# Performance work log

Measured on AMD Instinct MI355X. Metric: run time of the kernel, lower is better.

The kernel has to match this reference:

```python
import jax, jax.numpy as jnp
import numpy as np

N, K, C, H, V = 4096, 32, 128, 128, 21   # residues, kNN, node/edge dim, hidden, vocab
NEG_SLOPE = 0.2

def gatv2(src_feat, tgt_feat, edge_feat, Wl, bl, Wr, br, We, be, att, b_out):
    # GATv2Conv (1 head, eval mode) on a regular kNN graph.
    # src_feat: [N,K,Din] gathered source-node features per edge; tgt_feat: [N,Din]
    xl = src_feat @ Wl + bl                       # [N,K,C]
    xr = tgt_feat @ Wr + br                       # [N,C]
    ee = edge_feat @ We + be                      # [N,K,C]
    m = jax.nn.leaky_relu(xl + xr[:, None, :] + ee, NEG_SLOPE)
    alpha = jax.nn.softmax(jnp.einsum('nkc,c->nk', m, att), axis=1)
    return jnp.einsum('nk,nkc->nc', alpha, xl) + b_out

def setup_inputs():
    key = jax.random.key(0)
    ks = jax.random.split(key, 32)
    w = lambda k, s: jax.random.normal(k, s, jnp.float32) * 0.05
    z0 = lambda s: jnp.zeros(s, jnp.float32)
    return dict(
        E=jax.random.normal(ks[0], (N, K, C), jnp.float32),
        E_idx=jax.random.randint(ks[1], (N, K), 0, N),
        S=jax.random.randint(ks[2], (N,), 0, V),
        mask=jnp.ones((N,), jnp.float32),
        chain_M=jnp.ones((N,), jnp.float32),
        z=jax.random.normal(ks[3], (N,), jnp.float32),
        Wl1=w(ks[4], (C, C)), bl1=z0((C,)),
        Wr1=w(ks[5], (C, C)), br1=z0((C,)),
        We1=w(ks[6], (C, C)), be1=z0((C,)),
        a1=w(ks[7], (C,)), bo1=z0((C,)),
        Wl2=w(ks[8], (C + H, C)), bl2=z0((C,)),
        Wr2=w(ks[9], (C + H, C)), br2=z0((C,)),
        We2=w(ks[10], (C, C)), be2=z0((C,)),
        a2=w(ks[11], (C,)), bo2=z0((C,)),
        W_s=w(ks[12], (V, H)),
        W_out=w(ks[13], (C, V)), b_out=z0((V,)),
    )

def reference(E, E_idx, S, mask, chain_M, z,
              Wl1, bl1, Wr1, br1, We1, be1, a1, bo1,
              Wl2, bl2, Wr2, br2, We2, be2, a2, bo2,
              W_s, W_out, b_out):
    # encoder GAT over zero-initialized node features
    x0 = jnp.zeros((N, C), E.dtype)
    node_attr = gatv2(x0[E_idx], x0, E, Wl1, bl1, Wr1, br1, We1, be1, a1, bo1)
    seq_attr = W_s[S]                                        # [N,H]
    h_full = jnp.concatenate([node_attr, seq_attr], -1)      # [N,C+H]
    h_mask = jnp.concatenate([node_attr, jnp.zeros_like(seq_attr)], -1)
    cm = chain_M * mask
    decoding_order = jnp.argsort((cm + 1e-4) * jnp.abs(z))   # [N]
    P = jax.nn.one_hot(decoding_order, N, dtype=E.dtype)     # [N,N] permutation
    L = 1.0 - jnp.triu(jnp.ones((N, N), E.dtype))            # strictly lower tri
    order_mask_backward = jnp.einsum('ij,iq,jp->qp', L, P, P)
    mask_attend = jnp.take_along_axis(order_mask_backward, E_idx, axis=1)[..., None]
    m1d = mask[:, None, None]
    mask_bw = m1d * mask_attend
    mask_fw = m1d * (1.0 - mask_attend)
    # per-edge source features: neighbor seq embedding visible only if decoded earlier
    src = h_full[E_idx] * mask_bw + h_mask[E_idx] * mask_fw  # [N,K,C+H]
    out = gatv2(src, h_mask, E, Wl2, bl2, Wr2, br2, We2, be2, a2, bo2)
    logits = out @ W_out + b_out
    return jax.nn.log_softmax(logits, axis=-1)
```

## Files before the change

kernel.cpp:

```cpp
#include <hip/hip_runtime.h>
#include <hip/hip_bf16.h>

typedef short short8 __attribute__((ext_vector_type(8)));
typedef float float4v __attribute__((ext_vector_type(4)));

#define WS_T   0
#define WS_D   2688
#define WS_C   2816
#define WS_O   2944
#define WS_A2  3072
#define WS_G   7296
#define WS_B0  7744
#define WS_B1  7776
#define WS_M   7808

__device__ __forceinline__ unsigned int pack2bf(float a, float b) {
  union { float f; unsigned int u; } xa, xb;
  xa.f = a; xb.f = b;
  return ((xa.u + 0x8000u) >> 16) | ((xb.u + 0x8000u) & 0xFFFF0000u);
}

__global__ __launch_bounds__(256) void pg10_pre(
    const float* __restrict__ Wl2, const float* __restrict__ Wr2,
    const float* __restrict__ We2, const float* __restrict__ bl1,
    const float* __restrict__ bl2, const float* __restrict__ br2,
    const float* __restrict__ be2, const float* __restrict__ a2,
    const float* __restrict__ bo1, const float* __restrict__ bo2,
    const float* __restrict__ W_s, const float* __restrict__ mask,
    const float* __restrict__ chain_M, const float* __restrict__ z,
    const int* __restrict__ S, const float* __restrict__ W_out,
    const float* __restrict__ b_out, void* __restrict__ ws)
{
  __shared__ float sA[128], sB[128];
  short* wsW = (short*)ws;
  float* F = (float*)ws + 8192;
  const int b = blockIdx.x, tid = threadIdx.x;
  if (b == 0) {
    for (int s = tid; s < 16384; s += 256) {
      const int row = s >> 7, c = s & 127;
      const int q = row >> 5, lh = (row & 31) >> 3, j = row & 7;
      const int t = c >> 4, cl = c & 15;
      union { float f; unsigned int u; } x; x.f = We2[s];
      const unsigned int r = x.u + 0x7FFFu + ((x.u >> 16) & 1u);
      wsW[(((q * 8 + t) * 64) + lh * 16 + cl) * 8 + j] = (short)(r >> 16);
    }
    if (tid < 128) {
      const int c = tid;
      float cl0 = 0.f, cr0 = 0.f;
      for (int i = 0; i < 128; i++) {
        const float s = bl1[i] + bo1[i];
        cl0 += s * Wl2[i * 128 + c];
        cr0 += s * Wr2[i * 128 + c];
      }
      const float O = bl2[c] + bo2[c];
      F[WS_D + c]  = be2[c] + bl2[c] + br2[c] + cr0;
      F[WS_C + c]  = cl0;
      F[WS_O + c]  = O;
      F[WS_A2 + c] = a2[c];
      sA[c] = O;
      sB[c] = cl0;
    }
    __syncthreads();
    if (tid < 21) {
      float b0 = b_out[tid], b1 = 0.f;
      for (int c = 0; c < 128; c++) {
        b0 = fmaf(sA[c], W_out[c * 21 + tid], b0);
        b1 = fmaf(sB[c], W_out[c * 21 + tid], b1);
      }
      F[WS_B0 + tid] = b0;
      F[WS_B1 + tid] = b1;
    }
  } else if (b <= 21) {
    const int v = b - 1;
    if (tid < 128) {
      const int c = tid;
      float acc = 0.f;
      for (int h = 0; h < 128; h++)
        acc += W_s[v * 128 + h] * Wl2[(128 + h) * 128 + c];
      F[WS_T + v * 128 + c] = acc;
      sA[c] = acc;
    }
    __syncthreads();
    if (tid < 21) {
      float g = 0.f;
      for (int c = 0; c < 128; c++)
        g = fmaf(sA[c], W_out[c * 21 + tid], g);
      F[WS_G + v * 21 + tid] = g;
    }
  } else {
    const int n = (b - 22) * 256 + tid;
    F[WS_M + 2 * n] = (chain_M[n] * mask[n] + 1e-4f) * fabsf(z[n]);
    ((int*)F)[WS_M + 2 * n + 1] = S[n];
  }
}

__global__ __launch_bounds__(256, 4) void pg10_main(
    const float* __restrict__ E, const int* __restrict__ E_idx,
    const float* __restrict__ mask, const void* __restrict__ ws,
    float* __restrict__ out)
{
  __shared__ __align__(16) short ldsE[4][32 * 136];

  const short* wsW = (const short*)ws;
  const float* F = (const float*)ws + 8192;
  const int tid  = threadIdx.x;
  const int wave = tid >> 6;
  const int lane = tid & 63;
  const int quad = lane >> 4;
  const int lid  = lane & 15;
  const int n    = blockIdx.x * 4 + wave;
  const float maskn = mask[n];

  int jidx = 0;
  if (lane < 32) jidx = E_idx[n * 32 + lane];

  const float* ebase = E + (size_t)n * 32 * 128;
  short* myE = ldsE[wave];
#pragma unroll
  for (int i = 0; i < 8; i++) {
    const int e = i * 512 + lane * 8;
    const float4 A = *(const float4*)(ebase + e);
    const float4 B = *(const float4*)(ebase + e + 4);
    union { short8 s; unsigned int u[4]; } v;
    v.u[0] = pack2bf(A.x, A.y);
    v.u[1] = pack2bf(A.z, A.w);
    v.u[2] = pack2bf(B.x, B.y);
    v.u[3] = pack2bf(B.z, B.w);
    *(short8*)(myE + (e >> 7) * 136 + (e & 127)) = v.s;
  }

  float wkv = 0.f; int rvv = 0;
  const float keyn = F[WS_M + 2 * n];
  if (lane < 32) {
    const float2 mj = *(const float2*)(F + WS_M + 2 * jidx);
    const int before = (mj.x < keyn) || (mj.x == keyn && jidx < n);
    wkv = before ? maskn : 0.f;
    union { float f; int i; } c; c.f = mj.y; rvv = c.i;
  }
  int rows[2][4]; float wks[2][4];
#pragma unroll
  for (int g = 0; g < 2; g++)
#pragma unroll
    for (int r = 0; r < 4; r++) {
      const int kk = g * 16 + quad * 4 + r;
      rows[g][r] = __shfl(rvv, kk) * 128;
      wks[g][r]  = __shfl(wkv, kk);
    }

  __builtin_amdgcn_wave_barrier();

  short8 afr[2][4];
#pragma unroll
  for (int g = 0; g < 2; g++)
#pragma unroll
    for (int q = 0; q < 4; q++)
      afr[g][q] = *(const short8*)(myE + (g * 16 + lid) * 136 + q * 32 + quad * 8);

  float part[2][4] = {{0.f, 0.f, 0.f, 0.f}, {0.f, 0.f, 0.f, 0.f}};
#pragma unroll
  for (int t = 0; t < 8; t++) {
    short8 bfr[4];
#pragma unroll
    for (int q = 0; q < 4; q++)
      bfr[q] = *(const short8*)(wsW + (((q * 8 + t) * 64) + lane) * 8);
    float4v ac0 = {0.f, 0.f, 0.f, 0.f}, ac1 = {0.f, 0.f, 0.f, 0.f};
#pragma unroll
    for (int q = 0; q < 4; q++) {
      ac0 = __builtin_amdgcn_mfma_f32_16x16x32_bf16(afr[0][q], bfr[q], ac0, 0, 0, 0);
      ac1 = __builtin_amdgcn_mfma_f32_16x16x32_bf16(afr[1][q], bfr[q], ac1, 0, 0, 0);
    }
    const int c = t * 16 + lid;
    const float dvt  = F[WS_D + c] + maskn * F[WS_C + c];
    const float a2vt = F[WS_A2 + c];
#pragma unroll
    for (int r = 0; r < 4; r++) {
      float v0 = ac0[r] + dvt + wks[0][r] * F[WS_T + rows[0][r] + c];
      float v1 = ac1[r] + dvt + wks[1][r] * F[WS_T + rows[1][r] + c];
      v0 = fmaxf(v0, 0.f) + 0.2f * fminf(v0, 0.f);
      v1 = fmaxf(v1, 0.f) + 0.2f * fminf(v1, 0.f);
      part[0][r] = fmaf(v0, a2vt, part[0][r]);
      part[1][r] = fmaf(v1, a2vt, part[1][r]);
    }
  }
  float sreg[2][4];
#pragma unroll
  for (int g = 0; g < 2; g++)
#pragma unroll
    for (int r = 0; r < 4; r++) {
      float v = part[g][r];
      v += __shfl_xor(v, 1);
      v += __shfl_xor(v, 2);
      v += __shfl_xor(v, 4);
      v += __shfl_xor(v, 8);
      sreg[g][r] = v;
    }

  float mx = -1e30f;
#pragma unroll
  for (int g = 0; g < 2; g++)
#pragma unroll
    for (int r = 0; r < 4; r++) mx = fmaxf(mx, sreg[g][r]);
  mx = fmaxf(mx, __shfl_xor(mx, 16));
  mx = fmaxf(mx, __shfl_xor(mx, 32));
  float eg[2][4], esum = 0.f;
#pragma unroll
  for (int g = 0; g < 2; g++)
#pragma unroll
    for (int r = 0; r < 4; r++) {
      eg[g][r] = expf(sreg[g][r] - mx);
      esum += eg[g][r];
    }
  esum += __shfl_xor(esum, 16);
  esum += __shfl_xor(esum, 32);
  const float inv = 1.f / esum;
  float cg[2][4];
#pragma unroll
  for (int g = 0; g < 2; g++)
#pragma unroll
    for (int r = 0; r < 4; r++) cg[g][r] = eg[g][r] * inv * wks[g][r];

  float lg = (lane < 21) ? (F[WS_B0 + lane] + maskn * F[WS_B1 + lane]) : -1e30f;
#pragma unroll
  for (int kk = 0; kk < 32; kk++) {
    const int g = kk >> 4, sq = (kk >> 2) & 3, r = kk & 3;
    const float cf = __shfl(cg[g][r], sq * 16);
    const int row = (rows[0][0], __shfl(rvv, kk)) * 21;
    if (lane < 21) lg = fmaf(cf, F[WS_G + row + lane], lg);
  }

  float lmx = lg;
  lmx = fmaxf(lmx, __shfl_xor(lmx, 1));
  lmx = fmaxf(lmx, __shfl_xor(lmx, 2));
  lmx = fmaxf(lmx, __shfl_xor(lmx, 4));
  lmx = fmaxf(lmx, __shfl_xor(lmx, 8));
  lmx = fmaxf(lmx, __shfl_xor(lmx, 16));
  float ex = (lane < 21) ? expf(lg - lmx) : 0.f;
  float es = ex;
  es += __shfl_xor(es, 1);
  es += __shfl_xor(es, 2);
  es += __shfl_xor(es, 4);
  es += __shfl_xor(es, 8);
  es += __shfl_xor(es, 16);
  if (lane < 21)
    out[n * 21 + lane] = lg - lmx - logf(es);
}

extern "C" void kernel_launch(void* const* d_in, const int* in_sizes, int n_in,
                              void* d_out, int out_size, void* d_ws, size_t ws_size,
                              hipStream_t stream)
{
  const float* E       = (const float*)d_in[0];
  const int*   E_idx   = (const int*)d_in[1];
  const int*   S       = (const int*)d_in[2];
  const float* mask    = (const float*)d_in[3];
  const float* chain_M = (const float*)d_in[4];
  const float* z       = (const float*)d_in[5];
  const float* bl1     = (const float*)d_in[7];
  const float* bo1     = (const float*)d_in[13];
  const float* Wl2     = (const float*)d_in[14];
  const float* bl2     = (const float*)d_in[15];
  const float* Wr2     = (const float*)d_in[16];
  const float* br2     = (const float*)d_in[17];
  const float* We2     = (const float*)d_in[18];
  const float* be2     = (const float*)d_in[19];
  const float* a2      = (const float*)d_in[20];
  const float* bo2     = (const float*)d_in[21];
  const float* W_s     = (const float*)d_in[22];
  const float* W_out   = (const float*)d_in[23];
  const float* b_out   = (const float*)d_in[24];

  pg10_pre<<<38, 256, 0, stream>>>(Wl2, Wr2, We2, bl1, bl2, br2, be2, a2,
                                   bo1, bo2, W_s, mask, chain_M, z, S,
                                   W_out, b_out, d_ws);
  pg10_main<<<1024, 256, 0, stream>>>(E, E_idx, mask, d_ws, (float*)d_out);
}
```

Baseline: 168.2 us.

## Fuse preprocessing into main kernel with flag-based inter-block synchronization

Merges the weight-preprocessing kernel into the main GAT kernel. The first 38 blocks do the preprocessing and then publish release flags; every block spin-waits on those flags after staging its E tile into LDS. This removes a kernel launch and the inter-kernel gap, and lets the E loads overlap with the preprocessing. It also hoists the per-column bias and attention loads out of the MFMA loop, splits the logit accumulation into two chains, and uses the HIP bf16 pack intrinsic. The flags are never reset between calls, so later calls can read stale workspace without waiting, and correctness relies on the flag blocks being resident.

```diff
diff --git a/kernel.cpp b/kernel.cpp
--- a/kernel.cpp
+++ b/kernel.cpp
@@ -4,111 +4,120 @@
 typedef short short8 __attribute__((ext_vector_type(8)));
 typedef float float4v __attribute__((ext_vector_type(4)));
 
-#define WS_T   0
-#define WS_D   2688
-#define WS_C   2816
-#define WS_O   2944
-#define WS_A2  3072
-#define WS_G   7296
-#define WS_B0  7744
-#define WS_B1  7776
-#define WS_M   7808
-
-__device__ __forceinline__ unsigned int pack2bf(float a, float b) {
-  union { float f; unsigned int u; } xa, xb;
-  xa.f = a; xb.f = b;
-  return ((xa.u + 0x8000u) >> 16) | ((xb.u + 0x8000u) & 0xFFFF0000u);
+#define WS_T    0
+#define WS_D    2688
+#define WS_C    2816
+#define WS_O    2944
+#define WS_A2   3072
+#define WS_G    7296
+#define WS_B0   7744
+#define WS_B1   7776
+#define WS_M    7808
+#define WS_FLG  16000
+#define MAGIC   0x5EEDF00D
+
+__device__ __forceinline__ ushort f2bf(float f) {
+  union { float f; unsigned int u; } x;
+  x.f = f;
+  unsigned int r = x.u + 0x7FFFu + ((x.u >> 16) & 1u);
+  return (ushort)(r >> 16);
 }
-
-__global__ __launch_bounds__(256) void pg10_pre(
-    const float* __restrict__ Wl2, const float* __restrict__ Wr2,
-    const float* __restrict__ We2, const float* __restrict__ bl1,
-    const float* __restrict__ bl2, const float* __restrict__ br2,
-    const float* __restrict__ be2, const float* __restrict__ a2,
-    const float* __restrict__ bo1, const float* __restrict__ bo2,
-    const float* __restrict__ W_s, const float* __restrict__ mask,
+__device__ __forceinline__ unsigned int pkbf(float a, float b) {
+  __hip_bfloat162 h = __float22bfloat162_rn(make_float2(a, b));
+  return *(unsigned int*)&h;
+}
+
+__global__ __launch_bounds__(256, 4) void pg11(
+    const float* __restrict__ E, const int* __restrict__ E_idx,
+    const int* __restrict__ S, const float* __restrict__ mask,
     const float* __restrict__ chain_M, const float* __restrict__ z,
-    const int* __restrict__ S, const float* __restrict__ W_out,
-    const float* __restrict__ b_out, void* __restrict__ ws)
-{
-  __shared__ float sA[128], sB[128];
-  short* wsW = (short*)ws;
-  float* F = (float*)ws + 8192;
-  const int b = blockIdx.x, tid = threadIdx.x;
-  if (b == 0) {
-    for (int s = tid; s < 16384; s += 256) {
-      const int row = s >> 7, c = s & 127;
-      const int q = row >> 5, lh = (row & 31) >> 3, j = row & 7;
-      const int t = c >> 4, cl = c & 15;
-      union { float f; unsigned int u; } x; x.f = We2[s];
-      const unsigned int r = x.u + 0x7FFFu + ((x.u >> 16) & 1u);
-      wsW[(((q * 8 + t) * 64) + lh * 16 + cl) * 8 + j] = (short)(r >> 16);
-    }
-    if (tid < 128) {
-      const int c = tid;
-      float cl0 = 0.f, cr0 = 0.f;
-      for (int i = 0; i < 128; i++) {
-        const float s = bl1[i] + bo1[i];
-        cl0 += s * Wl2[i * 128 + c];
-        cr0 += s * Wr2[i * 128 + c];
-      }
-      const float O = bl2[c] + bo2[c];
-      F[WS_D + c]  = be2[c] + bl2[c] + br2[c] + cr0;
-      F[WS_C + c]  = cl0;
-      F[WS_O + c]  = O;
-      F[WS_A2 + c] = a2[c];
-      sA[c] = O;
-      sB[c] = cl0;
-    }
-    __syncthreads();
-    if (tid < 21) {
-      float b0 = b_out[tid], b1 = 0.f;
-      for (int c = 0; c < 128; c++) {
-        b0 = fmaf(sA[c], W_out[c * 21 + tid], b0);
-        b1 = fmaf(sB[c], W_out[c * 21 + tid], b1);
-      }
-      F[WS_B0 + tid] = b0;
-      F[WS_B1 + tid] = b1;
-    }
-  } else if (b <= 21) {
-    const int v = b - 1;
-    if (tid < 128) {
-      const int c = tid;
-      float acc = 0.f;
-      for (int h = 0; h < 128; h++)
-        acc += W_s[v * 128 + h] * Wl2[(128 + h) * 128 + c];
-      F[WS_T + v * 128 + c] = acc;
-      sA[c] = acc;
-    }
-    __syncthreads();
-    if (tid < 21) {
-      float g = 0.f;
-      for (int c = 0; c < 128; c++)
-        g = fmaf(sA[c], W_out[c * 21 + tid], g);
-      F[WS_G + v * 21 + tid] = g;
-    }
-  } else {
-    const int n = (b - 22) * 256 + tid;
-    F[WS_M + 2 * n] = (chain_M[n] * mask[n] + 1e-4f) * fabsf(z[n]);
-    ((int*)F)[WS_M + 2 * n + 1] = S[n];
-  }
-}
-
-__global__ __launch_bounds__(256, 4) void pg10_main(
-    const float* __restrict__ E, const int* __restrict__ E_idx,
-    const float* __restrict__ mask, const void* __restrict__ ws,
+    const float* __restrict__ bl1, const float* __restrict__ bo1,
+    const float* __restrict__ Wl2, const float* __restrict__ bl2,
+    const float* __restrict__ Wr2, const float* __restrict__ br2,
+    const float* __restrict__ We2, const float* __restrict__ be2,
+    const float* __restrict__ a2, const float* __restrict__ bo2,
+    const float* __restrict__ W_s, const float* __restrict__ W_out,
+    const float* __restrict__ b_out, void* __restrict__ ws,
     float* __restrict__ out)
 {
   __shared__ __align__(16) short ldsE[4][32 * 136];
-
-  const short* wsW = (const short*)ws;
-  const float* F = (const float*)ws + 8192;
-  const int tid  = threadIdx.x;
+  __shared__ float sA[128], sB[128];
+
+  short* wsW = (short*)ws;
+  float* F = (float*)ws + 8192;
+  int*   flg = (int*)(F + WS_FLG);
+  const int b   = blockIdx.x;
+  const int tid = threadIdx.x;
+
+  if (b < 38) {
+    if (b == 0) {
+      for (int s = tid; s < 16384; s += 256) {
+        const int row = s >> 7, c = s & 127;
+        const int q = row >> 5, lh = (row & 31) >> 3, j = row & 7;
+        const int t = c >> 4, cl = c & 15;
+        wsW[(((q * 8 + t) * 64) + lh * 16 + cl) * 8 + j] = (short)f2bf(We2[s]);
+      }
+      if (tid < 128) {
+        const int c = tid;
+        float cl0 = 0.f, cr0 = 0.f;
+        for (int i = 0; i < 128; i++) {
+          const float s = bl1[i] + bo1[i];
+          cl0 += s * Wl2[i * 128 + c];
+          cr0 += s * Wr2[i * 128 + c];
+        }
+        const float O = bl2[c] + bo2[c];
+        F[WS_D + c]  = be2[c] + bl2[c] + br2[c] + cr0;
+        F[WS_C + c]  = cl0;
+        F[WS_O + c]  = O;
+        F[WS_A2 + c] = a2[c];
+        sA[c] = O;
+        sB[c] = cl0;
+      }
+      __syncthreads();
+      if (tid < 21) {
+        float b0 = b_out[tid], b1 = 0.f;
+        for (int c = 0; c < 128; c++) {
+          b0 = fmaf(sA[c], W_out[c * 21 + tid], b0);
+          b1 = fmaf(sB[c], W_out[c * 21 + tid], b1);
+        }
+        F[WS_B0 + tid] = b0;
+        F[WS_B1 + tid] = b1;
+      }
+    } else if (b <= 21) {
+      const int v = b - 1;
+      if (tid < 128) {
+        const int c = tid;
+        float acc = 0.f;
+        for (int h = 0; h < 128; h++)
+          acc += W_s[v * 128 + h] * Wl2[(128 + h) * 128 + c];
+        F[WS_T + v * 128 + c] = acc;
+        sA[c] = acc;
+      }
+      __syncthreads();
+      if (tid < 21) {
+        float g = 0.f;
+        for (int c = 0; c < 128; c++)
+          g = fmaf(sA[c], W_out[c * 21 + tid], g);
+        F[WS_G + v * 21 + tid] = g;
+      }
+    } else {
+      const int n = (b - 22) * 256 + tid;
+      F[WS_M + 2 * n] = (chain_M[n] * mask[n] + 1e-4f) * fabsf(z[n]);
+      ((int*)F)[WS_M + 2 * n + 1] = S[n];
+    }
+    __syncthreads();
+    if (tid == 0) {
+      __threadfence();
+      __hip_atomic_store(&flg[b], MAGIC, __ATOMIC_RELEASE,
+                         __HIP_MEMORY_SCOPE_AGENT);
+    }
+  }
+
   const int wave = tid >> 6;
   const int lane = tid & 63;
   const int quad = lane >> 4;
   const int lid  = lane & 15;
-  const int n    = blockIdx.x * 4 + wave;
+  const int n    = b * 4 + wave;
   const float maskn = mask[n];
 
   int jidx = 0;
@@ -122,12 +131,20 @@
     const float4 A = *(const float4*)(ebase + e);
     const float4 B = *(const float4*)(ebase + e + 4);
     union { short8 s; unsigned int u[4]; } v;
-    v.u[0] = pack2bf(A.x, A.y);
-    v.u[1] = pack2bf(A.z, A.w);
-    v.u[2] = pack2bf(B.x, B.y);
-    v.u[3] = pack2bf(B.z, B.w);
+    v.u[0] = pkbf(A.x, A.y);
+    v.u[1] = pkbf(A.z, A.w);
+    v.u[2] = pkbf(B.x, B.y);
+    v.u[3] = pkbf(B.z, B.w);
     *(short8*)(myE + (e >> 7) * 136 + (e & 127)) = v.s;
   }
+
+  if (tid < 38) {
+    while (__hip_atomic_load(&flg[tid], __ATOMIC_ACQUIRE,
+                             __HIP_MEMORY_SCOPE_AGENT) != MAGIC)
+      __builtin_amdgcn_s_sleep(8);
+  }
+  __syncthreads();
+  __threadfence();
 
   float wkv = 0.f; int rvv = 0;
   const float keyn = F[WS_M + 2 * n];
@@ -147,7 +164,13 @@
       wks[g][r]  = __shfl(wkv, kk);
     }
 
-  __builtin_amdgcn_wave_barrier();
+  float dv[8], a2v[8];
+#pragma unroll
+  for (int t = 0; t < 8; t++) {
+    const int c = t * 16 + lid;
+    dv[t]  = F[WS_D + c] + maskn * F[WS_C + c];
+    a2v[t] = F[WS_A2 + c];
+  }
 
   short8 afr[2][4];
 #pragma unroll
@@ -170,16 +193,14 @@
       ac1 = __builtin_amdgcn_mfma_f32_16x16x32_bf16(afr[1][q], bfr[q], ac1, 0, 0, 0);
     }
     const int c = t * 16 + lid;
-    const float dvt  = F[WS_D + c] + maskn * F[WS_C + c];
-    const float a2vt = F[WS_A2 + c];
 #pragma unroll
     for (int r = 0; r < 4; r++) {
-      float v0 = ac0[r] + dvt + wks[0][r] * F[WS_T + rows[0][r] + c];
-      float v1 = ac1[r] + dvt + wks[1][r] * F[WS_T + rows[1][r] + c];
+      float v0 = ac0[r] + dv[t] + wks[0][r] * F[WS_T + rows[0][r] + c];
+      float v1 = ac1[r] + dv[t] + wks[1][r] * F[WS_T + rows[1][r] + c];
       v0 = fmaxf(v0, 0.f) + 0.2f * fminf(v0, 0.f);
       v1 = fmaxf(v1, 0.f) + 0.2f * fminf(v1, 0.f);
-      part[0][r] = fmaf(v0, a2vt, part[0][r]);
-      part[1][r] = fmaf(v1, a2vt, part[1][r]);
+      part[0][r] = fmaf(v0, a2v[t], part[0][r]);
+      part[1][r] = fmaf(v1, a2v[t], part[1][r]);
     }
   }
   float sreg[2][4];
@@ -219,14 +240,23 @@
 #pragma unroll
     for (int r = 0; r < 4; r++) cg[g][r] = eg[g][r] * inv * wks[g][r];
 
-  float lg = (lane < 21) ? (F[WS_B0 + lane] + maskn * F[WS_B1 + lane]) : -1e30f;
-#pragma unroll
-  for (int kk = 0; kk < 32; kk++) {
-    const int g = kk >> 4, sq = (kk >> 2) & 3, r = kk & 3;
-    const float cf = __shfl(cg[g][r], sq * 16);
-    const int row = (rows[0][0], __shfl(rvv, kk)) * 21;
-    if (lane < 21) lg = fmaf(cf, F[WS_G + row + lane], lg);
-  }
+  float lg0 = (lane < 21) ? (F[WS_B0 + lane] + maskn * F[WS_B1 + lane]) : -1e30f;
+  float lg1 = 0.f;
+#pragma unroll
+  for (int kk = 0; kk < 32; kk += 2) {
+    const int g0 = kk >> 4, sq0 = (kk >> 2) & 3, r0 = kk & 3;
+    const int k1 = kk + 1;
+    const int g1 = k1 >> 4, sq1 = (k1 >> 2) & 3, r1 = k1 & 3;
+    const float cf0 = __shfl(cg[g0][r0], sq0 * 16);
+    const float cf1 = __shfl(cg[g1][r1], sq1 * 16);
+    const int row0 = __shfl(rvv, kk) * 21;
+    const int row1 = __shfl(rvv, k1) * 21;
+    if (lane < 21) {
+      lg0 = fmaf(cf0, F[WS_G + row0 + lane], lg0);
+      lg1 = fmaf(cf1, F[WS_G + row1 + lane], lg1);
+    }
+  }
+  float lg = lg0 + lg1;
 
   float lmx = lg;
   lmx = fmaxf(lmx, __shfl_xor(lmx, 1));
@@ -249,28 +279,25 @@
                               void* d_out, int out_size, void* d_ws, size_t ws_size,
                               hipStream_t stream)
 {
-  const float* E       = (const float*)d_in[0];
-  const int*   E_idx   = (const int*)d_in[1];
-  const int*   S       = (const int*)d_in[2];
-  const float* mask    = (const float*)d_in[3];
-  const float* chain_M = (const float*)d_in[4];
-  const float* z       = (const float*)d_in[5];
-  const float* bl1     = (const float*)d_in[7];
-  const float* bo1     = (const float*)d_in[13];
-  const float* Wl2     = (const float*)d_in[14];
-  const float* bl2     = (const float*)d_in[15];
-  const float* Wr2     = (const float*)d_in[16];
-  const float* br2     = (const float*)d_in[17];
-  const float* We2     = (const float*)d_in[18];
-  const float* be2     = (const float*)d_in[19];
-  const float* a2      = (const float*)d_in[20];
-  const float* bo2     = (const float*)d_in[21];
-  const float* W_s     = (const float*)d_in[22];
-  const float* W_out   = (const float*)d_in[23];
-  const float* b_out   = (const float*)d_in[24];
-
-  pg10_pre<<<38, 256, 0, stream>>>(Wl2, Wr2, We2, bl1, bl2, br2, be2, a2,
-                                   bo1, bo2, W_s, mask, chain_M, z, S,
-                                   W_out, b_out, d_ws);
-  pg10_main<<<1024, 256, 0, stream>>>(E, E_idx, mask, d_ws, (float*)d_out);
+  pg11<<<1024, 256, 0, stream>>>(
+      (const float*)d_in[0],
+      (const int*)d_in[1],
+      (const int*)d_in[2],
+      (const float*)d_in[3],
+      (const float*)d_in[4],
+      (const float*)d_in[5],
+      (const float*)d_in[7],
+      (const float*)d_in[13],
+      (const float*)d_in[14],
+      (const float*)d_in[15],
+      (const float*)d_in[16],
+      (const float*)d_in[17],
+      (const float*)d_in[18],
+      (const float*)d_in[19],
+      (const float*)d_in[20],
+      (const float*)d_in[21],
+      (const float*)d_in[22],
+      (const float*)d_in[23],
+      (const float*)d_in[24],
+      d_ws, (float*)d_out);
 }
```

Measured after the change: 533.0 us. +216.9%, slower.
